# Kernel tuning notes

Hardware: AMD Instinct MI355X
Metric: run time of the kernel (lower is better)

The kernel has to match this reference:

```python
import jax, jax.numpy as jnp
import numpy as np

N = 50000      # nodes
E = 1600000    # edges
E_HIDDEN = 256
R_HIDDEN = 128
R = 1000       # number of relations (rel.max()+1)
EPS = 1e-16


def segment_softmax(scores, seg, num_segments):
    # numerically stable softmax over variable-size groups defined by seg
    m = jax.ops.segment_max(scores, seg, num_segments=num_segments)
    ex = jnp.exp(scores - m[seg])
    s = jax.ops.segment_sum(ex, seg, num_segments=num_segments)
    return ex / (s[seg] + EPS)


def setup_inputs() -> dict:
    key = jax.random.key(0)
    ks = jax.random.split(key, 9)
    x_e = jax.random.normal(ks[0], (N, E_HIDDEN), dtype=jnp.float32)
    edge_index = jax.random.randint(ks[1], (2, E), 0, N, dtype=jnp.int64)
    rel = jax.random.randint(ks[2], (E,), 0, R, dtype=jnp.int64)
    # learned params (Linear without bias); stored as [in, out]
    sc_w = 1.0 / np.sqrt(E_HIDDEN)
    sc_a = 1.0 / np.sqrt(R_HIDDEN)
    W_h = jax.random.uniform(ks[3], (E_HIDDEN, R_HIDDEN), jnp.float32, -sc_w, sc_w)
    W_t = jax.random.uniform(ks[4], (E_HIDDEN, R_HIDDEN), jnp.float32, -sc_w, sc_w)
    a_h1 = jax.random.uniform(ks[5], (R_HIDDEN,), jnp.float32, -sc_a, sc_a)
    a_h2 = jax.random.uniform(ks[6], (R_HIDDEN,), jnp.float32, -sc_a, sc_a)
    a_t1 = jax.random.uniform(ks[7], (R_HIDDEN,), jnp.float32, -sc_a, sc_a)
    a_t2 = jax.random.uniform(ks[8], (R_HIDDEN,), jnp.float32, -sc_a, sc_a)
    return {"x_e": x_e, "edge_index": edge_index, "rel": rel,
            "W_h": W_h, "W_t": W_t,
            "a_h1": a_h1, "a_h2": a_h2, "a_t1": a_t1, "a_t2": a_t2}


def reference(x_e, edge_index, rel, W_h, W_t, a_h1, a_h2, a_t1, a_t2):
    h_idx, t_idx = edge_index[0], edge_index[1]
    x_r_h = x_e @ W_h          # [N, r_hidden]
    x_r_t = x_e @ W_t          # [N, r_hidden]
    # per-node scalar scores, gathered per edge
    s_h1 = x_r_h @ a_h1        # [N]
    s_h2 = x_r_t @ a_h2
    s_t1 = x_r_h @ a_t1
    s_t2 = x_r_t @ a_t2
    e1 = s_h1[h_idx] + s_h2[t_idx]   # [E]
    e2 = s_t1[h_idx] + s_t2[t_idx]   # [E]
    alpha1 = segment_softmax(jax.nn.leaky_relu(e1, 0.01), rel, R)
    alpha2 = segment_softmax(jax.nn.leaky_relu(e2, 0.01), rel, R)
    # spmm: out[r] += alpha_e * feat[node_e]
    out_h = jax.ops.segment_sum(alpha1[:, None] * x_r_h[h_idx], rel, num_segments=R)
    out_t = jax.ops.segment_sum(alpha2[:, None] * x_r_t[t_idx], rel, num_segments=R)
    return out_h + out_t       # [R, r_hidden]
```

## Files before the change

### kernel.cpp

```cpp
#include <hip/hip_runtime.h>
#include <hip/hip_fp16.h>
#include <cstdint>
#include <cstddef>

#define E_HID 256
#define R_HID 128
#define NREL  1000
#define EPSF  1e-16f
#define NB    256
#define CH_BITS 12
#define NCH   13
#define NBIN  (NREL * NCH)
#define SPLIT 2
#define G5    (2 * NREL * SPLIT)

typedef _Float16 f16x8 __attribute__((ext_vector_type(8)));
typedef float f32x4 __attribute__((ext_vector_type(4)));

struct alignas(16) h8 { __half2 a, b, c, d; };

__global__ __launch_bounds__(256) void k0_prep(
    const float* __restrict__ Wh, const float* __restrict__ Wt,
    __half* __restrict__ WcT)
{
  const int k = blockIdx.x;
  const int c = threadIdx.x;
  const float v = (c < R_HID) ? Wh[(size_t)k * R_HID + c]
                              : Wt[(size_t)k * R_HID + (c - R_HID)];
  WcT[(size_t)c * E_HID + k] = __float2half(v);
}

__global__ __launch_bounds__(256) void k1_gemm(
    const float* __restrict__ xe, const __half* __restrict__ WcT,
    const float* __restrict__ ah1, const float* __restrict__ ah2,
    const float* __restrict__ at1, const float* __restrict__ at2,
    __half* __restrict__ xhH, __half* __restrict__ xtH,
    float* __restrict__ sh1, float* __restrict__ sh2,
    float* __restrict__ st1, float* __restrict__ st2, int N)
{
  __shared__ __half As[128 * 32];
  __shared__ __half Bs[128 * 32];
  __shared__ float sA[2][128];
  __shared__ float sB[2][128];

  const int tid  = threadIdx.x;
  const int lane = tid & 63;
  const int wid  = tid >> 6;
  const int wr = wid >> 1, wc = wid & 1;
  const int nbm = (N + 127) >> 7;
  const int mb = blockIdx.x % nbm;
  const int cb = blockIdx.x / nbm;
  const int n0 = mb * 128;

  f32x4 acc[4][4];
  #pragma unroll
  for (int m = 0; m < 4; ++m)
    #pragma unroll
    for (int n = 0; n < 4; ++n) acc[m][n] = (f32x4){0.f, 0.f, 0.f, 0.f};

  const int arow = tid >> 1, ah = tid & 1;
  const bool aok = (n0 + arow) < N;
  const float*  xsrc = xe + (size_t)(n0 + arow) * E_HID + ah * 16;
  const __half* bsrc = WcT + ((size_t)(cb * 128 + arow) << 8) + ah * 16;
  __half* Aw = &As[arow * 32 + ah * 16];
  __half* Bw = &Bs[arow * 32 + ah * 16];

  const int fr = lane & 15, fq = lane >> 4;

  for (int kt = 0; kt < 8; ++kt) {
    __syncthreads();
    float4 v0 = make_float4(0,0,0,0), v1 = v0, v2 = v0, v3 = v0;
    if (aok) {
      const float* s = xsrc + kt * 32;
      v0 = *(const float4*)(s);     v1 = *(const float4*)(s + 4);
      v2 = *(const float4*)(s + 8); v3 = *(const float4*)(s + 12);
    }
    h8 p0, p1;
    p0.a = __floats2half2_rn(v0.x, v0.y); p0.b = __floats2half2_rn(v0.z, v0.w);
    p0.c = __floats2half2_rn(v1.x, v1.y); p0.d = __floats2half2_rn(v1.z, v1.w);
    p1.a = __floats2half2_rn(v2.x, v2.y); p1.b = __floats2half2_rn(v2.z, v2.w);
    p1.c = __floats2half2_rn(v3.x, v3.y); p1.d = __floats2half2_rn(v3.z, v3.w);
    *(h8*)(Aw) = p0; *(h8*)(Aw + 8) = p1;
    float4 b0 = *(const float4*)(bsrc + kt * 32);
    float4 b1 = *(const float4*)(bsrc + kt * 32 + 8);
    *(float4*)(Bw) = b0; *(float4*)(Bw + 8) = b1;
    __syncthreads();
    f16x8 aF[4], bF[4];
    #pragma unroll
    for (int m = 0; m < 4; ++m)
      aF[m] = *(const f16x8*)&As[(wr * 64 + m * 16 + fr) * 32 + fq * 8];
    #pragma unroll
    for (int n = 0; n < 4; ++n)
      bF[n] = *(const f16x8*)&Bs[(wc * 64 + n * 16 + fr) * 32 + fq * 8];
    #pragma unroll
    for (int m = 0; m < 4; ++m)
      #pragma unroll
      for (int n = 0; n < 4; ++n)
        acc[m][n] = __builtin_amdgcn_mfma_f32_16x16x32_f16(aF[m], bF[n], acc[m][n], 0, 0, 0);
  }

  __half* dst = (cb == 0) ? xhH : xtH;
  #pragma unroll
  for (int m = 0; m < 4; ++m) {
    const int rl0 = wr * 64 + m * 16 + fq * 4;
    #pragma unroll
    for (int r = 0; r < 4; ++r) {
      const int node = n0 + rl0 + r;
      if (node < N) {
        #pragma unroll
        for (int n = 0; n < 4; ++n)
          dst[(size_t)node * R_HID + wc * 64 + n * 16 + fr] = __float2half(acc[m][n][r]);
      }
    }
  }

  const float* aV1 = (cb == 0) ? ah1 : ah2;
  const float* aV2 = (cb == 0) ? at1 : at2;
  float avA[4], avB[4];
  #pragma unroll
  for (int n = 0; n < 4; ++n) {
    avA[n] = aV1[wc * 64 + n * 16 + fr];
    avB[n] = aV2[wc * 64 + n * 16 + fr];
  }
  #pragma unroll
  for (int m = 0; m < 4; ++m)
    #pragma unroll
    for (int r = 0; r < 4; ++r) {
      float vA = acc[m][0][r]*avA[0] + acc[m][1][r]*avA[1]
               + acc[m][2][r]*avA[2] + acc[m][3][r]*avA[3];
      float vB = acc[m][0][r]*avB[0] + acc[m][1][r]*avB[1]
               + acc[m][2][r]*avB[2] + acc[m][3][r]*avB[3];
      #pragma unroll
      for (int ofs = 1; ofs < 16; ofs <<= 1) {
        vA += __shfl_xor(vA, ofs, 16);
        vB += __shfl_xor(vB, ofs, 16);
      }
      if (fr == 0) {
        const int rl = wr * 64 + m * 16 + fq * 4 + r;
        sA[wc][rl] = vA;
        sB[wc][rl] = vB;
      }
    }
  __syncthreads();
  if (tid < 128 && n0 + tid < N) {
    float* o1 = (cb == 0) ? sh1 : sh2;
    float* o2 = (cb == 0) ? st1 : st2;
    o1[n0 + tid] = sA[0][tid] + sA[1][tid];
    o2[n0 + tid] = sB[0][tid] + sB[1][tid];
  }
}

__global__ __launch_bounds__(256) void k2_hist(
    const int* __restrict__ ei, const int* __restrict__ rel,
    unsigned short* __restrict__ bc, int E)
{
  __shared__ unsigned lc[NBIN];
  const int tid  = threadIdx.x;
  const int list = blockIdx.x / NB;
  const int b    = blockIdx.x % NB;
  for (int j = tid; j < NBIN; j += 256) lc[j] = 0u;
  __syncthreads();
  const int* nodes = ei + (size_t)list * E;
  for (int i = b * 256 + tid; i < E; i += NB * 256)
    atomicAdd(&lc[rel[i] * NCH + (nodes[i] >> CH_BITS)], 1u);
  __syncthreads();
  unsigned short* dst = bc + ((size_t)(list * NB + b)) * NBIN;
  for (int j = tid; j < NBIN; j += 256) dst[j] = (unsigned short)lc[j];
}

__global__ __launch_bounds__(64) void k3a_scan(
    const unsigned short* __restrict__ bc, unsigned short* __restrict__ pre,
    unsigned* __restrict__ cnt)
{
  const int list = blockIdx.x / NBIN;
  const int bin  = blockIdx.x % NBIN;
  const int lane = threadIdx.x;
  unsigned running = 0u;
  for (int b0 = 0; b0 < NB; b0 += 64) {
    const int b = b0 + lane;
    const size_t idx = ((size_t)(list * NB + b)) * NBIN + bin;
    const unsigned v = bc[idx];
    unsigned inc = v;
    #pragma unroll
    for (int ofs = 1; ofs < 64; ofs <<= 1) {
      const unsigned nv = __shfl_up(inc, ofs, 64);
      if (lane >= ofs) inc += nv;
    }
    pre[idx] = (unsigned short)(running + inc - v);
    running += __shfl(inc, 63, 64);
  }
  if (lane == 0) cnt[list * NBIN + bin] = running;
}

__global__ __launch_bounds__(1024) void k3b_scan(
    const unsigned* __restrict__ cnt, unsigned* __restrict__ offs)
{
  __shared__ unsigned s[1024];
  const int t = threadIdx.x;
  for (int list = 0; list < 2; ++list) {
    const unsigned* c = cnt + (size_t)list * NBIN;
    unsigned* o = offs + (size_t)list * (NBIN + 1);
    unsigned carry = 0u;
    for (int base = 0; base < NBIN; base += 1024) {
      const int idx = base + t;
      const unsigned v = (idx < NBIN) ? c[idx] : 0u;
      s[t] = v;
      __syncthreads();
      for (int ofs = 1; ofs < 1024; ofs <<= 1) {
        const unsigned add = (t >= ofs) ? s[t - ofs] : 0u;
        __syncthreads();
        s[t] += add;
        __syncthreads();
      }
      if (idx < NBIN) o[idx] = carry + s[t] - v;
      carry += s[1023];
      __syncthreads();
    }
    if (t == 0) o[NBIN] = carry;
    __syncthreads();
  }
}

__global__ __launch_bounds__(256) void k4_scatter(
    const int* __restrict__ ei, const int* __restrict__ rel,
    const float* __restrict__ sh1, const float* __restrict__ sh2,
    const float* __restrict__ st1, const float* __restrict__ st2,
    const unsigned* __restrict__ offs, const unsigned short* __restrict__ pre,
    uint2* __restrict__ metaH, uint2* __restrict__ metaT, int E)
{
  __shared__ unsigned lb[NBIN];
  const int tid  = threadIdx.x;
  const int list = blockIdx.x / NB;
  const int b    = blockIdx.x % NB;
  const unsigned* o = offs + (size_t)list * (NBIN + 1);
  const unsigned short* pr = pre + ((size_t)(list * NB + b)) * NBIN;
  for (int j = tid; j < NBIN; j += 256) lb[j] = o[j] + pr[j];
  __syncthreads();
  uint2* meta = list ? metaT : metaH;
  for (int i = b * 256 + tid; i < E; i += NB * 256) {
    const int h = ei[i], t = ei[E + i], r = rel[i];
    float e, node;
    int nd;
    if (list == 0) { e = sh1[h] + sh2[t]; nd = h; }
    else           { e = st1[h] + st2[t]; nd = t; }
    const float l = e >= 0.f ? e : 0.01f * e;
    const float w = expf(l);
    const unsigned pos = atomicAdd(&lb[r * NCH + (nd >> CH_BITS)], 1u);
    meta[pos] = make_uint2((unsigned)nd, __float_as_uint(w));
    (void)node;
  }
}

__global__ __launch_bounds__(256) void k5_reduce(
    const unsigned* __restrict__ offs,
    const uint2* __restrict__ metaH, const uint2* __restrict__ metaT,
    const __half* __restrict__ xhH, const __half* __restrict__ xtH,
    float* __restrict__ part, float* __restrict__ partS)
{
  __shared__ float accW[4][130];
  __shared__ float accSw[4];
  const int tid  = threadIdx.x;
  const int lane = tid & 63;
  const int wv   = __builtin_amdgcn_readfirstlane(tid >> 6);
  const int bid  = blockIdx.x;
  const int list = bid / (NREL * SPLIT);
  const int rr   = bid % (NREL * SPLIT);
  const int r    = rr / SPLIT;
  const int sp   = rr % SPLIT;

  const unsigned* o    = offs + (size_t)list * (NBIN + 1);
  const uint2*    meta = list ? metaT : metaH;
  const __half*   xsrc = list ? xtH   : xhH;
  const __half*   xl   = xsrc + 2 * lane;

  const unsigned R0 = o[r * NCH];
  const unsigned R1 = o[r * NCH + NCH];
  const unsigned len = R1 - R0;
  const int q = sp * 4 + wv;
  unsigned p        = R0 + (unsigned)(((unsigned long long)len * (unsigned)q) >> 3);
  const unsigned pe = R0 + (unsigned)(((unsigned long long)len * (unsigned)(q + 1)) >> 3);

  float a0 = 0.f, a1 = 0.f, sw = 0.f;

  for (; p + 4 <= pe; p += 4) {
    const uint2 m0 = meta[p],     m1 = meta[p + 1];
    const uint2 m2 = meta[p + 2], m3 = meta[p + 3];
    const float2 f0 = __half22float2(*(const __half2*)(xl + ((size_t)m0.x << 7)));
    const float2 f1 = __half22float2(*(const __half2*)(xl + ((size_t)m1.x << 7)));
    const float2 f2 = __half22float2(*(const __half2*)(xl + ((size_t)m2.x << 7)));
    const float2 f3 = __half22float2(*(const __half2*)(xl + ((size_t)m3.x << 7)));
    const float w0 = __uint_as_float(m0.y), w1 = __uint_as_float(m1.y);
    const float w2 = __uint_as_float(m2.y), w3 = __uint_as_float(m3.y);
    a0 += w0 * f0.x; a1 += w0 * f0.y; sw += w0;
    a0 += w1 * f1.x; a1 += w1 * f1.y; sw += w1;
    a0 += w2 * f2.x; a1 += w2 * f2.y; sw += w2;
    a0 += w3 * f3.x; a1 += w3 * f3.y; sw += w3;
  }
  for (; p < pe; ++p) {
    const uint2 m = meta[p];
    const float2 f = __half22float2(*(const __half2*)(xl + ((size_t)m.x << 7)));
    const float w = __uint_as_float(m.y);
    a0 += w * f.x; a1 += w * f.y; sw += w;
  }

  accW[wv][2 * lane]     = a0;
  accW[wv][2 * lane + 1] = a1;
  if (lane == 0) accSw[wv] = sw;
  __syncthreads();
  if (tid < 128) {
    const float v = accW[0][tid] + accW[1][tid] + accW[2][tid] + accW[3][tid];
    part[(size_t)bid * R_HID + tid] = v;
  }
  if (tid == 0)
    partS[bid] = accSw[0] + accSw[1] + accSw[2] + accSw[3];
}

__global__ __launch_bounds__(128) void k6_final(
    const float* __restrict__ part, const float* __restrict__ partS,
    float* __restrict__ out)
{
  const int r = blockIdx.x;
  const int d = threadIdx.x;
  float oh = 0.f, ot = 0.f, s1 = 0.f, s2 = 0.f;
  #pragma unroll
  for (int sp = 0; sp < SPLIT; ++sp) {
    const int pid0 = r * SPLIT + sp;
    const int pid1 = (NREL + r) * SPLIT + sp;
    oh += part[(size_t)pid0 * R_HID + d];
    ot += part[(size_t)pid1 * R_HID + d];
    s1 += partS[pid0];
    s2 += partS[pid1];
  }
  out[r * R_HID + d] = oh / (s1 + EPSF) + ot / (s2 + EPSF);
}

extern "C" void kernel_launch(void* const* d_in, const int* in_sizes, int n_in,
                              void* d_out, int out_size, void* d_ws, size_t ws_size,
                              hipStream_t stream) {
  const float* xe  = (const float*)d_in[0];
  const int*   ei  = (const int*)d_in[1];
  const int*   rel = (const int*)d_in[2];
  const float* Wh  = (const float*)d_in[3];
  const float* Wt  = (const float*)d_in[4];
  const float* ah1 = (const float*)d_in[5];
  const float* ah2 = (const float*)d_in[6];
  const float* at1 = (const float*)d_in[7];
  const float* at2 = (const float*)d_in[8];
  const int N = in_sizes[0] / E_HID;
  const int E = in_sizes[2];

  char* w = (char*)d_ws;
  size_t o = 0;
  auto alloc = [&](size_t bytes) -> void* {
    void* p = w + o;
    o = (o + bytes + 255) & ~(size_t)255;
    return p;
  };
  __half* WcT = (__half*)alloc((size_t)E_HID * E_HID * 2);
  __half* xhH = (__half*)alloc((size_t)N * R_HID * 2);
  __half* xtH = (__half*)alloc((size_t)N * R_HID * 2);
  float* sh1 = (float*)alloc((size_t)N * 4);
  float* sh2 = (float*)alloc((size_t)N * 4);
  float* st1 = (float*)alloc((size_t)N * 4);
  float* st2 = (float*)alloc((size_t)N * 4);
  uint2* metaH = (uint2*)alloc((size_t)E * 8);
  uint2* metaT = (uint2*)alloc((size_t)E * 8);
  unsigned short* bc  = (unsigned short*)alloc((size_t)2 * NB * NBIN * 2);
  unsigned short* pre = (unsigned short*)alloc((size_t)2 * NB * NBIN * 2);
  unsigned* cnt  = (unsigned*)alloc((size_t)2 * NBIN * 4);
  unsigned* offs = (unsigned*)alloc((size_t)2 * (NBIN + 1) * 4);
  float* part  = (float*)alloc((size_t)G5 * R_HID * 4);
  float* partS = (float*)alloc((size_t)G5 * 4);

  const int nbm = (N + 127) >> 7;
  k0_prep<<<E_HID, 256, 0, stream>>>(Wh, Wt, WcT);
  k1_gemm<<<nbm * 2, 256, 0, stream>>>(xe, WcT, ah1, ah2, at1, at2,
                                       xhH, xtH, sh1, sh2, st1, st2, N);
  k2_hist<<<2 * NB, 256, 0, stream>>>(ei, rel, bc, E);
  k3a_scan<<<2 * NBIN, 64, 0, stream>>>(bc, pre, cnt);
  k3b_scan<<<1, 1024, 0, stream>>>(cnt, offs);
  k4_scatter<<<2 * NB, 256, 0, stream>>>(ei, rel, sh1, sh2, st1, st2,
                                         offs, pre, metaH, metaT, E);
  k5_reduce<<<G5, 256, 0, stream>>>(offs, metaH, metaT, xhH, xtH, part, partS);
  k6_final<<<NREL, 128, 0, stream>>>(part, partS, (float*)d_out);
}
```

Before: 305.4 us.

## Replace per-block histogram bucketing with global atomic counting sort

```diff
diff --git a/kernel.cpp b/kernel.cpp
--- a/kernel.cpp
+++ b/kernel.cpp
@@ -7,12 +7,10 @@
 #define R_HID 128
 #define NREL  1000
 #define EPSF  1e-16f
-#define NB    256
-#define CH_BITS 12
-#define NCH   13
+#define CH_BITS 11
+#define NCH   25
 #define NBIN  (NREL * NCH)
-#define SPLIT 2
-#define G5    (2 * NREL * SPLIT)
+#define G5    (2 * NREL)
 
 typedef _Float16 f16x8 __attribute__((ext_vector_type(8)));
 typedef float f32x4 __attribute__((ext_vector_type(4)));
@@ -152,102 +150,67 @@
 
 __global__ __launch_bounds__(256) void k2_hist(
     const int* __restrict__ ei, const int* __restrict__ rel,
-    unsigned short* __restrict__ bc, int E)
-{
-  __shared__ unsigned lc[NBIN];
-  const int tid  = threadIdx.x;
-  const int list = blockIdx.x / NB;
-  const int b    = blockIdx.x % NB;
-  for (int j = tid; j < NBIN; j += 256) lc[j] = 0u;
-  __syncthreads();
-  const int* nodes = ei + (size_t)list * E;
-  for (int i = b * 256 + tid; i < E; i += NB * 256)
-    atomicAdd(&lc[rel[i] * NCH + (nodes[i] >> CH_BITS)], 1u);
-  __syncthreads();
-  unsigned short* dst = bc + ((size_t)(list * NB + b)) * NBIN;
-  for (int j = tid; j < NBIN; j += 256) dst[j] = (unsigned short)lc[j];
-}
-
-__global__ __launch_bounds__(64) void k3a_scan(
-    const unsigned short* __restrict__ bc, unsigned short* __restrict__ pre,
-    unsigned* __restrict__ cnt)
-{
-  const int list = blockIdx.x / NBIN;
-  const int bin  = blockIdx.x % NBIN;
-  const int lane = threadIdx.x;
-  unsigned running = 0u;
-  for (int b0 = 0; b0 < NB; b0 += 64) {
-    const int b = b0 + lane;
-    const size_t idx = ((size_t)(list * NB + b)) * NBIN + bin;
-    const unsigned v = bc[idx];
-    unsigned inc = v;
-    #pragma unroll
-    for (int ofs = 1; ofs < 64; ofs <<= 1) {
-      const unsigned nv = __shfl_up(inc, ofs, 64);
-      if (lane >= ofs) inc += nv;
-    }
-    pre[idx] = (unsigned short)(running + inc - v);
-    running += __shfl(inc, 63, 64);
-  }
-  if (lane == 0) cnt[list * NBIN + bin] = running;
-}
-
-__global__ __launch_bounds__(1024) void k3b_scan(
-    const unsigned* __restrict__ cnt, unsigned* __restrict__ offs)
+    unsigned* __restrict__ cntH, unsigned* __restrict__ cntT, int E)
+{
+  for (int i = blockIdx.x * 256 + threadIdx.x; i < E; i += gridDim.x * 256) {
+    const int r = rel[i];
+    atomicAdd(cntH + r * NCH + (ei[i] >> CH_BITS), 1u);
+    atomicAdd(cntT + r * NCH + (ei[E + i] >> CH_BITS), 1u);
+  }
+}
+
+__global__ __launch_bounds__(1024) void k3_scan(
+    const unsigned* __restrict__ cnt, unsigned* __restrict__ offs,
+    unsigned* __restrict__ cur)
 {
   __shared__ unsigned s[1024];
+  const int list = blockIdx.x;
+  const unsigned* c = cnt + (size_t)list * NBIN;
+  unsigned* o = offs + (size_t)list * (NBIN + 1);
+  unsigned* u = cur  + (size_t)list * NBIN;
   const int t = threadIdx.x;
-  for (int list = 0; list < 2; ++list) {
-    const unsigned* c = cnt + (size_t)list * NBIN;
-    unsigned* o = offs + (size_t)list * (NBIN + 1);
-    unsigned carry = 0u;
-    for (int base = 0; base < NBIN; base += 1024) {
-      const int idx = base + t;
-      const unsigned v = (idx < NBIN) ? c[idx] : 0u;
-      s[t] = v;
+  unsigned carry = 0u;
+  for (int base = 0; base < NBIN; base += 1024) {
+    const int idx = base + t;
+    const unsigned v = (idx < NBIN) ? c[idx] : 0u;
+    s[t] = v;
+    __syncthreads();
+    for (int ofs = 1; ofs < 1024; ofs <<= 1) {
+      const unsigned add = (t >= ofs) ? s[t - ofs] : 0u;
       __syncthreads();
-      for (int ofs = 1; ofs < 1024; ofs <<= 1) {
-        const unsigned add = (t >= ofs) ? s[t - ofs] : 0u;
-        __syncthreads();
-        s[t] += add;
-        __syncthreads();
-      }
-      if (idx < NBIN) o[idx] = carry + s[t] - v;
-      carry += s[1023];
+      s[t] += add;
       __syncthreads();
     }
-    if (t == 0) o[NBIN] = carry;
+    if (idx < NBIN) {
+      const unsigned e = carry + s[t] - v;
+      o[idx] = e;
+      u[idx] = e;
+    }
+    carry += s[1023];
     __syncthreads();
   }
+  if (t == 0) o[NBIN] = carry;
 }
 
 __global__ __launch_bounds__(256) void k4_scatter(
     const int* __restrict__ ei, const int* __restrict__ rel,
     const float* __restrict__ sh1, const float* __restrict__ sh2,
     const float* __restrict__ st1, const float* __restrict__ st2,
-    const unsigned* __restrict__ offs, const unsigned short* __restrict__ pre,
+    unsigned* __restrict__ curH, unsigned* __restrict__ curT,
     uint2* __restrict__ metaH, uint2* __restrict__ metaT, int E)
 {
-  __shared__ unsigned lb[NBIN];
-  const int tid  = threadIdx.x;
-  const int list = blockIdx.x / NB;
-  const int b    = blockIdx.x % NB;
-  const unsigned* o = offs + (size_t)list * (NBIN + 1);
-  const unsigned short* pr = pre + ((size_t)(list * NB + b)) * NBIN;
-  for (int j = tid; j < NBIN; j += 256) lb[j] = o[j] + pr[j];
-  __syncthreads();
-  uint2* meta = list ? metaT : metaH;
-  for (int i = b * 256 + tid; i < E; i += NB * 256) {
+  for (int i = blockIdx.x * 256 + threadIdx.x; i < E; i += gridDim.x * 256) {
     const int h = ei[i], t = ei[E + i], r = rel[i];
-    float e, node;
-    int nd;
-    if (list == 0) { e = sh1[h] + sh2[t]; nd = h; }
-    else           { e = st1[h] + st2[t]; nd = t; }
-    const float l = e >= 0.f ? e : 0.01f * e;
-    const float w = expf(l);
-    const unsigned pos = atomicAdd(&lb[r * NCH + (nd >> CH_BITS)], 1u);
-    meta[pos] = make_uint2((unsigned)nd, __float_as_uint(w));
-    (void)node;
+    const float e1 = sh1[h] + sh2[t];
+    const float e2 = st1[h] + st2[t];
+    const float l1 = e1 >= 0.f ? e1 : 0.01f * e1;
+    const float l2 = e2 >= 0.f ? e2 : 0.01f * e2;
+    const float w1 = expf(l1);
+    const float w2 = expf(l2);
+    const unsigned pH = atomicAdd(curH + r * NCH + (h >> CH_BITS), 1u);
+    metaH[pH] = make_uint2((unsigned)h, __float_as_uint(w1));
+    const unsigned pT = atomicAdd(curT + r * NCH + (t >> CH_BITS), 1u);
+    metaT[pT] = make_uint2((unsigned)t, __float_as_uint(w2));
   }
 }
 
@@ -263,44 +226,43 @@
   const int lane = tid & 63;
   const int wv   = __builtin_amdgcn_readfirstlane(tid >> 6);
   const int bid  = blockIdx.x;
-  const int list = bid / (NREL * SPLIT);
-  const int rr   = bid % (NREL * SPLIT);
-  const int r    = rr / SPLIT;
-  const int sp   = rr % SPLIT;
+  const int list = bid / NREL;
+  const int r    = bid % NREL;
 
   const unsigned* o    = offs + (size_t)list * (NBIN + 1);
   const uint2*    meta = list ? metaT : metaH;
   const __half*   xsrc = list ? xtH   : xhH;
   const __half*   xl   = xsrc + 2 * lane;
 
-  const unsigned R0 = o[r * NCH];
-  const unsigned R1 = o[r * NCH + NCH];
-  const unsigned len = R1 - R0;
-  const int q = sp * 4 + wv;
-  unsigned p        = R0 + (unsigned)(((unsigned long long)len * (unsigned)q) >> 3);
-  const unsigned pe = R0 + (unsigned)(((unsigned long long)len * (unsigned)(q + 1)) >> 3);
-
   float a0 = 0.f, a1 = 0.f, sw = 0.f;
 
-  for (; p + 4 <= pe; p += 4) {
-    const uint2 m0 = meta[p],     m1 = meta[p + 1];
-    const uint2 m2 = meta[p + 2], m3 = meta[p + 3];
-    const float2 f0 = __half22float2(*(const __half2*)(xl + ((size_t)m0.x << 7)));
-    const float2 f1 = __half22float2(*(const __half2*)(xl + ((size_t)m1.x << 7)));
-    const float2 f2 = __half22float2(*(const __half2*)(xl + ((size_t)m2.x << 7)));
-    const float2 f3 = __half22float2(*(const __half2*)(xl + ((size_t)m3.x << 7)));
-    const float w0 = __uint_as_float(m0.y), w1 = __uint_as_float(m1.y);
-    const float w2 = __uint_as_float(m2.y), w3 = __uint_as_float(m3.y);
-    a0 += w0 * f0.x; a1 += w0 * f0.y; sw += w0;
-    a0 += w1 * f1.x; a1 += w1 * f1.y; sw += w1;
-    a0 += w2 * f2.x; a1 += w2 * f2.y; sw += w2;
-    a0 += w3 * f3.x; a1 += w3 * f3.y; sw += w3;
-  }
-  for (; p < pe; ++p) {
-    const uint2 m = meta[p];
-    const float2 f = __half22float2(*(const __half2*)(xl + ((size_t)m.x << 7)));
-    const float w = __uint_as_float(m.y);
-    a0 += w * f.x; a1 += w * f.y; sw += w;
+  for (int c = 0; c < NCH; ++c) {
+    const unsigned s0 = o[r * NCH + c];
+    const unsigned s1 = o[r * NCH + c + 1];
+    const unsigned len = s1 - s0;
+    unsigned p        = s0 + ((len * (unsigned)wv) >> 2);
+    const unsigned pe = s0 + ((len * (unsigned)(wv + 1)) >> 2);
+
+    for (; p + 4 <= pe; p += 4) {
+      const uint2 m0 = meta[p],     m1 = meta[p + 1];
+      const uint2 m2 = meta[p + 2], m3 = meta[p + 3];
+      const float2 f0 = __half22float2(*(const __half2*)(xl + ((size_t)m0.x << 7)));
+      const float2 f1 = __half22float2(*(const __half2*)(xl + ((size_t)m1.x << 7)));
+      const float2 f2 = __half22float2(*(const __half2*)(xl + ((size_t)m2.x << 7)));
+      const float2 f3 = __half22float2(*(const __half2*)(xl + ((size_t)m3.x << 7)));
+      const float w0 = __uint_as_float(m0.y), w1 = __uint_as_float(m1.y);
+      const float w2 = __uint_as_float(m2.y), w3 = __uint_as_float(m3.y);
+      a0 += w0 * f0.x; a1 += w0 * f0.y; sw += w0;
+      a0 += w1 * f1.x; a1 += w1 * f1.y; sw += w1;
+      a0 += w2 * f2.x; a1 += w2 * f2.y; sw += w2;
+      a0 += w3 * f3.x; a1 += w3 * f3.y; sw += w3;
+    }
+    for (; p < pe; ++p) {
+      const uint2 m = meta[p];
+      const float2 f = __half22float2(*(const __half2*)(xl + ((size_t)m.x << 7)));
+      const float w = __uint_as_float(m.y);
+      a0 += w * f.x; a1 += w * f.y; sw += w;
+    }
   }
 
   accW[wv][2 * lane]     = a0;
@@ -308,8 +270,8 @@
   if (lane == 0) accSw[wv] = sw;
   __syncthreads();
   if (tid < 128) {
-    const float v = accW[0][tid] + accW[1][tid] + accW[2][tid] + accW[3][tid];
-    part[(size_t)bid * R_HID + tid] = v;
+    part[(size_t)bid * R_HID + tid] =
+        accW[0][tid] + accW[1][tid] + accW[2][tid] + accW[3][tid];
   }
   if (tid == 0)
     partS[bid] = accSw[0] + accSw[1] + accSw[2] + accSw[3];
@@ -321,16 +283,10 @@
 {
   const int r = blockIdx.x;
   const int d = threadIdx.x;
-  float oh = 0.f, ot = 0.f, s1 = 0.f, s2 = 0.f;
-  #pragma unroll
-  for (int sp = 0; sp < SPLIT; ++sp) {
-    const int pid0 = r * SPLIT + sp;
-    const int pid1 = (NREL + r) * SPLIT + sp;
-    oh += part[(size_t)pid0 * R_HID + d];
-    ot += part[(size_t)pid1 * R_HID + d];
-    s1 += partS[pid0];
-    s2 += partS[pid1];
-  }
+  const float oh = part[(size_t)r * R_HID + d];
+  const float ot = part[(size_t)(NREL + r) * R_HID + d];
+  const float s1 = partS[r];
+  const float s2 = partS[NREL + r];
   out[r * R_HID + d] = oh / (s1 + EPSF) + ot / (s2 + EPSF);
 }
 
@@ -365,22 +321,24 @@
   float* st2 = (float*)alloc((size_t)N * 4);
   uint2* metaH = (uint2*)alloc((size_t)E * 8);
   uint2* metaT = (uint2*)alloc((size_t)E * 8);
-  unsigned short* bc  = (unsigned short*)alloc((size_t)2 * NB * NBIN * 2);
-  unsigned short* pre = (unsigned short*)alloc((size_t)2 * NB * NBIN * 2);
-  unsigned* cnt  = (unsigned*)alloc((size_t)2 * NBIN * 4);
+  unsigned* cur  = (unsigned*)alloc((size_t)2 * NBIN * 4);
   unsigned* offs = (unsigned*)alloc((size_t)2 * (NBIN + 1) * 4);
   float* part  = (float*)alloc((size_t)G5 * R_HID * 4);
   float* partS = (float*)alloc((size_t)G5 * 4);
+  const size_t zstart = o;
+  unsigned* cnt  = (unsigned*)alloc((size_t)2 * NBIN * 4);
+  const size_t zbytes = o - zstart;
+
+  hipMemsetAsync(w + zstart, 0, zbytes, stream);
 
   const int nbm = (N + 127) >> 7;
   k0_prep<<<E_HID, 256, 0, stream>>>(Wh, Wt, WcT);
   k1_gemm<<<nbm * 2, 256, 0, stream>>>(xe, WcT, ah1, ah2, at1, at2,
                                        xhH, xtH, sh1, sh2, st1, st2, N);
-  k2_hist<<<2 * NB, 256, 0, stream>>>(ei, rel, bc, E);
-  k3a_scan<<<2 * NBIN, 64, 0, stream>>>(bc, pre, cnt);
-  k3b_scan<<<1, 1024, 0, stream>>>(cnt, offs);
-  k4_scatter<<<2 * NB, 256, 0, stream>>>(ei, rel, sh1, sh2, st1, st2,
-                                         offs, pre, metaH, metaT, E);
+  k2_hist<<<1024, 256, 0, stream>>>(ei, rel, cnt, cnt + NBIN, E);
+  k3_scan<<<2, 1024, 0, stream>>>(cnt, offs, cur);
+  k4_scatter<<<1024, 256, 0, stream>>>(ei, rel, sh1, sh2, st1, st2,
+                                       cur, cur + NBIN, metaH, metaT, E);
   k5_reduce<<<G5, 256, 0, stream>>>(offs, metaH, metaT, xhH, xtH, part, partS);
   k6_final<<<NREL, 128, 0, stream>>>(part, partS, (float*)d_out);
 }
```

Result: slower. 475.7 us (+55.8%).
